# Kernel tuning notes

Hardware: AMD Instinct MI355X
Metric: run time of the kernel (lower is better)

## Reference

```python
import jax, jax.numpy as jnp
import numpy as np

D_MODEL = 1024
N_HEADS = 16
D_FF = 4096
EPS = 1e-6


def layernorm(x, alpha, bias):
    # torch.std uses Bessel correction (ddof=1)
    mean = jnp.mean(x, axis=-1, keepdims=True)
    std = jnp.std(x, axis=-1, keepdims=True, ddof=1)
    return alpha * (x - mean) / (std + EPS) + bias


def setup_inputs() -> dict:
    key = jax.random.key(0)
    ks = jax.random.split(key, 12)
    s = 1.0 / np.sqrt(D_MODEL)
    sf = 1.0 / np.sqrt(D_FF)
    return {
        "x": jax.random.normal(ks[0], (2, 2048, D_MODEL), jnp.float32),
        "mask": jnp.ones((2, 1, 1, 2048), jnp.int32),
        "wq": jax.random.normal(ks[1], (D_MODEL, D_MODEL), jnp.float32) * s,
        "wk": jax.random.normal(ks[2], (D_MODEL, D_MODEL), jnp.float32) * s,
        "wv": jax.random.normal(ks[3], (D_MODEL, D_MODEL), jnp.float32) * s,
        "wo": jax.random.normal(ks[4], (D_MODEL, D_MODEL), jnp.float32) * s,
        "wo_b": jnp.zeros((D_MODEL,), jnp.float32),
        "w1": jax.random.normal(ks[5], (D_MODEL, D_FF), jnp.float32) * s,
        "b1": jnp.zeros((D_FF,), jnp.float32),
        "w2": jax.random.normal(ks[6], (D_FF, D_MODEL), jnp.float32) * sf,
        "b2": jnp.zeros((D_MODEL,), jnp.float32),
        "alpha1": jnp.ones((D_MODEL,), jnp.float32),
        "bias1": jnp.zeros((D_MODEL,), jnp.float32),
        "alpha2": jnp.ones((D_MODEL,), jnp.float32),
        "bias2": jnp.zeros((D_MODEL,), jnp.float32),
    }


def reference(x, mask, wq, wk, wv, wo, wo_b, w1, b1, w2, b2,
              alpha1, bias1, alpha2, bias2):
    B, S, D = x.shape
    h, dk = N_HEADS, D_MODEL // N_HEADS
    # projections -> [B, h, S, dk]
    q = (x @ wq).reshape(B, S, h, dk).transpose(0, 2, 1, 3)
    k = (x @ wk).reshape(B, S, h, dk).transpose(0, 2, 1, 3)
    v = (x @ wv).reshape(B, S, h, dk).transpose(0, 2, 1, 3)
    scores = jnp.einsum('bhqd,bhkd->bhqk', q, k) / jnp.sqrt(jnp.float32(dk))
    scores = jnp.where(mask == 0, jnp.float32(-1e9), scores)
    attn = jax.nn.softmax(scores, axis=-1)
    ctx = jnp.einsum('bhqk,bhkd->bhqd', attn, v)
    ctx = ctx.transpose(0, 2, 1, 3).reshape(B, S, D)
    attn_out = ctx @ wo + wo_b
    x = layernorm(x + attn_out, alpha1, bias1)
    ff = jax.nn.relu(x @ w1 + b1) @ w2 + b2
    x = layernorm(x + ff, alpha2, bias2)
    return x
```

## Files before the change

kernel.cpp:

```cpp
#include <hip/hip_runtime.h>
#include <hip/hip_bf16.h>

#define D_MODEL 1024
#define N_HEADS 16
#define DK      64
#define SEQ     2048
#define BATCH   2
#define D_FF    4096
#define ROWS    (BATCH*SEQ)
#define LN_EPS  1e-6f
#define SSTR    72
#define KTILE   128
#define PSTR    136

typedef __hip_bfloat16 bf16;
typedef __attribute__((ext_vector_type(8))) short frag8;
typedef __attribute__((ext_vector_type(4))) float facc4;

__device__ inline float bf2f(unsigned short u){ return __uint_as_float(((unsigned)u) << 16); }
__device__ inline float toF(bf16 v){ return __bfloat162float(v); }
__device__ inline unsigned short f2bu(float f){ bf16 h = __float2bfloat16(f); return *reinterpret_cast<unsigned short*>(&h); }

__device__ inline float ld1(const void* p, size_t idx, bool f32) {
    return f32 ? ((const float*)p)[idx] : toF(((const bf16*)p)[idx]);
}

struct U8 { unsigned short v[8]; };
__device__ inline U8 ld8bf(const void* p, size_t idx, bool f32) {
    U8 r;
    if (!f32) {
        *reinterpret_cast<uint4*>(r.v) = *reinterpret_cast<const uint4*>((const unsigned short*)p + idx);
    } else {
        const float* f = (const float*)p + idx;
        const float4 a = *reinterpret_cast<const float4*>(f);
        const float4 b = *reinterpret_cast<const float4*>(f + 4);
        r.v[0]=f2bu(a.x); r.v[1]=f2bu(a.y); r.v[2]=f2bu(a.z); r.v[3]=f2bu(a.w);
        r.v[4]=f2bu(b.x); r.v[5]=f2bu(b.y); r.v[6]=f2bu(b.z); r.v[7]=f2bu(b.w);
    }
    return r;
}

__device__ inline void gld16(const void* g, void* l) {
    __builtin_amdgcn_global_load_lds(
        reinterpret_cast<const __attribute__((address_space(1))) void*>(
            reinterpret_cast<uintptr_t>(g)),
        reinterpret_cast<__attribute__((address_space(3))) void*>(
            (unsigned int)reinterpret_cast<uintptr_t>(l)),
        16, 0, 0);
}

__global__ void probe_kernel(const void* __restrict__ xp, int* __restrict__ flag) {
    __shared__ int hit;
    if (threadIdx.x == 0) hit = 0;
    __syncthreads();
    const bf16* p = (const bf16*)xp;
    int bad = 0;
    for (int i = threadIdx.x; i < 8192; i += 256) {
        float v = fabsf(toF(p[i]));
        if (!(v <= 1e5f)) bad = 1;
    }
    if (bad) atomicOr(&hit, 1);
    __syncthreads();
    if (threadIdx.x == 0) *flag = hit;
}

__global__ __launch_bounds__(256) void xcvt_kernel(const void* __restrict__ x,
    bf16* __restrict__ out, const int* __restrict__ flagp)
{
    const bool f32 = (*flagp) != 0;
    const size_t i = ((size_t)blockIdx.x * 256 + threadIdx.x) * 8;
    U8 d = ld8bf(x, i, f32);
    *reinterpret_cast<uint4*>(out + i) = *reinterpret_cast<const uint4*>(d.v);
}

__global__ __launch_bounds__(256) void transpose_kernel(const void* __restrict__ W,
    bf16* __restrict__ WT, int K, int N, const int* __restrict__ flagp)
{
    const bool f32 = (*flagp) != 0;
    __shared__ float tile[32][33];
    const int tx = threadIdx.x, ty = threadIdx.y;
    const int n0 = blockIdx.x * 32, k0 = blockIdx.y * 32;
    #pragma unroll
    for (int r = 0; r < 4; ++r)
        tile[ty + 8*r][tx] = ld1(W, (size_t)(k0 + ty + 8*r) * N + n0 + tx, f32);
    __syncthreads();
    #pragma unroll
    for (int r = 0; r < 4; ++r)
        WT[(size_t)(n0 + ty + 8*r) * K + k0 + tx] = __float2bfloat16(tile[tx][ty + 8*r]);
}

__global__ __launch_bounds__(256) void transpose4_kernel(const void* __restrict__ w0,
    const void* __restrict__ w1, const void* __restrict__ w2, const void* __restrict__ w3,
    bf16* __restrict__ WT4, const int* __restrict__ flagp)
{
    const bool f32 = (*flagp) != 0;
    const int which = blockIdx.z;
    const void* W = (which == 0) ? w0 : (which == 1) ? w1 : (which == 2) ? w2 : w3;
    bf16* WT = WT4 + (size_t)which * D_MODEL * D_MODEL;
    __shared__ float tile[32][33];
    const int tx = threadIdx.x, ty = threadIdx.y;
    const int n0 = blockIdx.x * 32, k0 = blockIdx.y * 32;
    #pragma unroll
    for (int r = 0; r < 4; ++r)
        tile[ty + 8*r][tx] = ld1(W, (size_t)(k0 + ty + 8*r) * D_MODEL + n0 + tx, f32);
    __syncthreads();
    #pragma unroll
    for (int r = 0; r < 4; ++r)
        WT[(size_t)(n0 + ty + 8*r) * D_MODEL + k0 + tx] = __float2bfloat16(tile[tx][ty + 8*r]);
}

__global__ __launch_bounds__(256) void vtrans_kernel(const bf16* __restrict__ V,
    bf16* __restrict__ VT)
{
    __shared__ unsigned short tile[32][33];
    const int tx = threadIdx.x, ty = threadIdx.y;
    const int s0 = blockIdx.x * 32, d0 = blockIdx.y * 32;
    const int bh = blockIdx.z, b = bh >> 4, h = bh & 15;
    #pragma unroll
    for (int r = 0; r < 4; ++r)
        tile[ty + 8*r][tx] = *reinterpret_cast<const unsigned short*>(
            V + ((size_t)(b * SEQ + s0 + ty + 8*r)) * D_MODEL + h * DK + d0 + tx);
    __syncthreads();
    #pragma unroll
    for (int r = 0; r < 4; ++r)
        *reinterpret_cast<unsigned short*>(
            VT + ((size_t)(bh * DK + d0 + ty + 8*r)) * SEQ + s0 + tx) = tile[tx][ty + 8*r];
}

template<bool RELU, bool BIAS, int NMAT, int SPLITK>
__global__ __launch_bounds__(256) void mgemm_kernel(const bf16* __restrict__ A,
    const bf16* __restrict__ BT, const void* __restrict__ bias,
    bf16* __restrict__ C, int M, int N, int K, const int* __restrict__ flagp)
{
    const bool inF32 = (*flagp) != 0;

    __shared__ unsigned short sA[128 * 64];
    __shared__ unsigned short sB[128 * 64];

    int which = 0, colb = blockIdx.x;
    if (NMAT > 1) { which = blockIdx.x >> 3; colb = blockIdx.x & 7; }
    const int kslice = (SPLITK > 1) ? blockIdx.z : 0;
    const int Kspan  = K / SPLITK;
    const int kbase  = kslice * Kspan;
    const bf16* Bp = BT + (size_t)which * N * K;
    bf16*       Cp = C  + (size_t)which * M * N + (size_t)kslice * M * N;

    const int row0 = blockIdx.y * 128;
    const int col0 = colb * 128;

    const int t    = threadIdx.x;
    const int wave = t >> 6;
    const int lane = t & 63;
    const int lm   = lane & 15;
    const int q    = lane >> 4;
    const int wm   = (wave & 1) * 64;
    const int wn   = (wave >> 1) * 64;

    facc4 acc[4][4];
    #pragma unroll
    for (int i = 0; i < 4; ++i)
        #pragma unroll
        for (int j = 0; j < 4; ++j)
            acc[i][j] = (facc4){0.f, 0.f, 0.f, 0.f};

    for (int k0 = kbase; k0 < kbase + Kspan; k0 += 64) {
        __syncthreads();
        #pragma unroll
        for (int j = 0; j < 4; ++j) {
            const int ch = (wave * 4 + j) * 64 + lane;
            const int r  = ch >> 3;
            const int cs = ch & 7;
            const int c  = cs ^ (r & 7);
            gld16(A  + (size_t)(row0 + r) * K + k0 + 8 * c, &sA[(wave * 4 + j) * 512]);
            gld16(Bp + (size_t)(col0 + r) * K + k0 + 8 * c, &sB[(wave * 4 + j) * 512]);
        }
        __syncthreads();

        #pragma unroll
        for (int kk = 0; kk < 64; kk += 32) {
            const int cr = (kk >> 3) + q;
            frag8 af[4], bfr[4];
            #pragma unroll
            for (int im = 0; im < 4; ++im) {
                const int m = wm + 16 * im + lm;
                af[im] = *reinterpret_cast<const frag8*>(&sA[m * 64 + ((cr ^ (m & 7)) << 3)]);
            }
            #pragma unroll
            for (int in = 0; in < 4; ++in) {
                const int n = wn + 16 * in + lm;
                bfr[in] = *reinterpret_cast<const frag8*>(&sB[n * 64 + ((cr ^ (n & 7)) << 3)]);
            }
            #pragma unroll
            for (int im = 0; im < 4; ++im)
                #pragma unroll
                for (int in = 0; in < 4; ++in)
                    acc[im][in] = __builtin_amdgcn_mfma_f32_16x16x32_bf16(af[im], bfr[in], acc[im][in], 0, 0, 0);
        }
    }

    #pragma unroll
    for (int in = 0; in < 4; ++in) {
        const int col = col0 + wn + 16*in + lm;
        float bv = 0.f;
        if (BIAS && kslice == 0) bv = ld1(bias, col, inF32);
        #pragma unroll
        for (int im = 0; im < 4; ++im) {
            #pragma unroll
            for (int r = 0; r < 4; ++r) {
                const int row = row0 + wm + 16*im + 4*q + r;
                float v = acc[im][in][r] + bv;
                if (RELU) v = fmaxf(v, 0.f);
                Cp[(size_t)row * N + col] = __float2bfloat16(v);
            }
        }
    }
}

__global__ __launch_bounds__(512) void fattn_kernel(
    const bf16* __restrict__ Qg, const bf16* __restrict__ Kg,
    const bf16* __restrict__ VTg, const int* __restrict__ mask,
    bf16* __restrict__ ctx)
{
    __shared__ unsigned short sK[128 * 64];
    __shared__ unsigned short sV[64 * 128];
    __shared__ unsigned short PsU[8 * 16 * PSTR];
    __shared__ float madd[KTILE];

    const int t    = threadIdx.x;
    const int qt   = blockIdx.x;
    const int h    = blockIdx.y;
    const int b    = blockIdx.z;
    const int q0   = qt * 128;
    const int bh   = b * N_HEADS + h;
    const int wave = t >> 6;
    const int lane = t & 63;
    const int lm   = lane & 15;
    const int qd   = lane >> 4;

    unsigned short* Qs = PsU;
    {
        const int sr = t >> 2, sd0 = (t & 3) * 16;
        const unsigned short* src = (const unsigned short*)
            (Qg + ((size_t)(b * SEQ + q0 + sr)) * D_MODEL + h * DK + sd0);
        unsigned short qi[16], qo[16];
        *reinterpret_cast<uint4*>(&qi[0]) = *reinterpret_cast<const uint4*>(src);
        *reinterpret_cast<uint4*>(&qi[8]) = *reinterpret_cast<const uint4*>(src + 8);
        #pragma unroll
        for (int u = 0; u < 16; ++u) qo[u] = f2bu(bf2f(qi[u]) * 0.125f);
        *reinterpret_cast<uint4*>(&Qs[sr * SSTR + sd0])     = *reinterpret_cast<const uint4*>(&qo[0]);
        *reinterpret_cast<uint4*>(&Qs[sr * SSTR + sd0 + 8]) = *reinterpret_cast<const uint4*>(&qo[8]);
    }
    __syncthreads();
    frag8 qf[2];
    #pragma unroll
    for (int s2 = 0; s2 < 2; ++s2)
        qf[s2] = *reinterpret_cast<const frag8*>(&Qs[(16 * wave + lm) * SSTR + 32 * s2 + 8 * qd]);

    facc4 accO[4];
    float m_r[4], l_r[4];
    #pragma unroll
    for (int r = 0; r < 4; ++r) { m_r[r] = -1e30f; l_r[r] = 0.f; }
    #pragma unroll
    for (int in = 0; in < 4; ++in) accO[in] = (facc4){0.f, 0.f, 0.f, 0.f};

    for (int kt = 0; kt < SEQ / KTILE; ++kt) {
        const int k0 = kt * KTILE;
        __syncthreads();

        #pragma unroll
        for (int j = 0; j < 2; ++j) {
            const int ch = (wave * 2 + j) * 64 + lane;
            const int rK = ch >> 3, cK = (ch & 7) ^ (rK & 7);
            gld16(Kg + ((size_t)(b * SEQ + k0 + rK)) * D_MODEL + h * DK + 8 * cK,
                  &sK[(wave * 2 + j) * 512]);
            const int rV = ch >> 4, cV = (ch & 15) ^ (rV & 15);
            gld16(VTg + ((size_t)(bh * DK + rV)) * SEQ + k0 + 8 * cV,
                  &sV[(wave * 2 + j) * 512]);
        }
        if (t < KTILE) madd[t] = (mask[b * SEQ + k0 + t] == 0) ? -1e9f : 0.f;
        __syncthreads();

        facc4 accS[8];
        #pragma unroll
        for (int i = 0; i < 8; ++i) accS[i] = (facc4){0.f, 0.f, 0.f, 0.f};
        #pragma unroll
        for (int i = 0; i < 8; ++i) {
            #pragma unroll
            for (int s2 = 0; s2 < 2; ++s2) {
                const int cr = 4 * s2 + qd;
                frag8 kf = *reinterpret_cast<const frag8*>(
                    &sK[(16 * i + lm) * 64 + ((cr ^ (lm & 7)) << 3)]);
                accS[i] = __builtin_amdgcn_mfma_f32_16x16x32_bf16(qf[s2], kf, accS[i], 0, 0, 0);
            }
        }

        float madv[8];
        #pragma unroll
        for (int i = 0; i < 8; ++i) madv[i] = madd[16 * i + lm];

        float mx[4];
        #pragma unroll
        for (int r = 0; r < 4; ++r) {
            float m0 = -1e30f;
            #pragma unroll
            for (int i = 0; i < 8; ++i) m0 = fmaxf(m0, accS[i][r] + madv[i]);
            #pragma unroll
            for (int off = 1; off < 16; off <<= 1) m0 = fmaxf(m0, __shfl_xor(m0, off));
            mx[r] = m0;
        }

        float alpha[4], mn[4], psum[4];
        #pragma unroll
        for (int r = 0; r < 4; ++r) {
            mn[r] = fmaxf(m_r[r], mx[r]);
            alpha[r] = __expf(m_r[r] - mn[r]);
            m_r[r] = mn[r];
            psum[r] = 0.f;
        }
        unsigned short* Pw = &PsU[wave * 16 * PSTR];
        #pragma unroll
        for (int i = 0; i < 8; ++i) {
            #pragma unroll
            for (int r = 0; r < 4; ++r) {
                float p = __expf(accS[i][r] + madv[i] - mn[r]);
                psum[r] += p;
                Pw[(qd * 4 + r) * PSTR + 16 * i + lm] = f2bu(p);
            }
        }
        #pragma unroll
        for (int r = 0; r < 4; ++r) {
            float s = psum[r];
            #pragma unroll
            for (int off = 1; off < 16; off <<= 1) s += __shfl_xor(s, off);
            l_r[r] = l_r[r] * alpha[r] + s;
            #pragma unroll
            for (int in = 0; in < 4; ++in) accO[in][r] *= alpha[r];
        }

        #pragma unroll
        for (int c = 0; c < 4; ++c) {
            frag8 pf = *reinterpret_cast<const frag8*>(&Pw[lm * PSTR + 32 * c + 8 * qd]);
            #pragma unroll
            for (int in = 0; in < 4; ++in) {
                const int cr = 4 * c + qd;
                frag8 vf = *reinterpret_cast<const frag8*>(
                    &sV[(16 * in + lm) * 128 + ((cr ^ lm) << 3)]);
                accO[in] = __builtin_amdgcn_mfma_f32_16x16x32_bf16(pf, vf, accO[in], 0, 0, 0);
            }
        }
    }

    float inv[4];
    #pragma unroll
    for (int r = 0; r < 4; ++r) inv[r] = 1.f / l_r[r];
    #pragma unroll
    for (int in = 0; in < 4; ++in)
        #pragma unroll
        for (int r = 0; r < 4; ++r)
            ctx[((size_t)(b * SEQ + q0 + 16 * wave + qd * 4 + r)) * D_MODEL + h * DK + 16 * in + lm]
                = __float2bfloat16(accO[in][r] * inv[r]);
}

template<bool BASE_WS, bool OUT_WS>
__global__ __launch_bounds__(256) void ln_kernel(const void* __restrict__ base,
    const bf16* __restrict__ addv, const bf16* __restrict__ addv2,
    const void* __restrict__ alpha, const void* __restrict__ bias,
    void* __restrict__ outp, const int* __restrict__ flagp)
{
    const bool inF32 = (*flagp) != 0;
    __shared__ float vals[D_MODEL];
    __shared__ float red[256];
    const int row = blockIdx.x, tid = threadIdx.x;

    float lsum = 0.f;
    for (int i = tid; i < D_MODEL; i += 256) {
        const size_t off = (size_t)row * D_MODEL + i;
        float v = (BASE_WS ? toF(((const bf16*)base)[off]) : ld1(base, off, inF32)) + toF(addv[off]);
        if (addv2) v += toF(addv2[off]);
        vals[i] = v; lsum += v;
    }
    red[tid] = lsum; __syncthreads();
    for (int s = 128; s > 0; s >>= 1) { if (tid < s) red[tid] += red[tid + s]; __syncthreads(); }
    const float mean = red[0] / (float)D_MODEL; __syncthreads();

    float lsq = 0.f;
    for (int i = tid; i < D_MODEL; i += 256) { float dd = vals[i] - mean; lsq += dd * dd; }
    red[tid] = lsq; __syncthreads();
    for (int s = 128; s > 0; s >>= 1) { if (tid < s) red[tid] += red[tid + s]; __syncthreads(); }
    const float var = red[0] / (float)(D_MODEL - 1);
    const float inv = 1.f / (sqrtf(var) + LN_EPS);

    for (int i = tid; i < D_MODEL; i += 256) {
        const size_t off = (size_t)row * D_MODEL + i;
        const float y = ld1(alpha, i, inF32) * (vals[i] - mean) * inv + ld1(bias, i, inF32);
        if (OUT_WS || !inF32) ((bf16*)outp)[off] = __float2bfloat16(y);
        else                  ((float*)outp)[off] = y;
    }
}

extern "C" void kernel_launch(void* const* d_in, const int* in_sizes, int n_in,
                              void* d_out, int out_size, void* d_ws, size_t ws_size,
                              hipStream_t stream)
{
    const void* x    = d_in[0];
    const int*  mask = (const int*)d_in[1];
    const void* wq   = d_in[2];
    const void* wk   = d_in[3];
    const void* wv   = d_in[4];
    const void* wo   = d_in[5];
    const void* wo_b = d_in[6];
    const void* w1   = d_in[7];
    const void* b1   = d_in[8];
    const void* w2   = d_in[9];
    const void* b2   = d_in[10];
    const void* al1  = d_in[11];
    const void* bi1  = d_in[12];
    const void* al2  = d_in[13];
    const void* bi2  = d_in[14];

    const size_t MB = 1024 * 1024;
    char* ws = (char*)d_ws;
    const bool BIG = ws_size >= 64 * MB + 4096;
    if (!BIG && ws_size < 56 * MB + 4096) return;

    dim3 tb(32, 8);

    if (BIG) {
        bf16* Qb   = (bf16*)(ws + 0 * MB);
        bf16* Kb   = (bf16*)(ws + 8 * MB);
        bf16* Vb   = (bf16*)(ws + 16 * MB);
        bf16* Xb   = (bf16*)(ws + 24 * MB);
        bf16* VTb  = (bf16*)(ws + 24 * MB);
        bf16* WT4  = (bf16*)(ws + 32 * MB);
        bf16* WOT  = WT4 + (size_t)3 * D_MODEL * D_MODEL;
        bf16* W1T  = (bf16*)(ws + 40 * MB);
        bf16* W2T  = (bf16*)(ws + 48 * MB);
        bf16* CTXb = (bf16*)(ws + 56 * MB);
        bf16* ATT0 = (bf16*)(ws + 0 * MB);
        bf16* ATT1 = (bf16*)(ws + 8 * MB);
        bf16* X1b  = (bf16*)(ws + 56 * MB);
        bf16* FFb  = (bf16*)(ws + 0 * MB);
        bf16* X20  = (bf16*)(ws + 32 * MB);
        bf16* X21  = (bf16*)(ws + 40 * MB);
        int*  flagp = (int*)(ws + 64 * MB);

        probe_kernel<<<1, 256, 0, stream>>>(x, flagp);
        xcvt_kernel<<<dim3(ROWS * D_MODEL / 2048), 256, 0, stream>>>(x, Xb, flagp);

        transpose4_kernel<<<dim3(32, 32, 4), tb, 0, stream>>>(wq, wk, wv, wo, WT4, flagp);
        transpose_kernel<<<dim3(128, 32), tb, 0, stream>>>(w1, W1T, D_MODEL, D_FF, flagp);
        transpose_kernel<<<dim3(32, 128), tb, 0, stream>>>(w2, W2T, D_FF, D_MODEL, flagp);

        mgemm_kernel<false, false, 3, 1><<<dim3(24, 32), 256, 0, stream>>>(
            Xb, WT4, nullptr, Qb, ROWS, D_MODEL, D_MODEL, flagp);

        vtrans_kernel<<<dim3(SEQ / 32, 2, BATCH * N_HEADS), tb, 0, stream>>>(Vb, VTb);

        fattn_kernel<<<dim3(SEQ / 128, N_HEADS, BATCH), 512, 0, stream>>>(Qb, Kb, VTb, mask, CTXb);

        mgemm_kernel<false, true, 1, 2><<<dim3(8, 32, 2), 256, 0, stream>>>(
            CTXb, WOT, wo_b, ATT0, ROWS, D_MODEL, D_MODEL, flagp);
        ln_kernel<false, true><<<ROWS, 256, 0, stream>>>(x, ATT0, ATT1, al1, bi1, X1b, flagp);

        mgemm_kernel<true, true, 1, 1><<<dim3(32, 32), 256, 0, stream>>>(
            X1b, W1T, b1, FFb, ROWS, D_FF, D_MODEL, flagp);

        mgemm_kernel<false, true, 1, 2><<<dim3(8, 32, 2), 256, 0, stream>>>(
            FFb, W2T, b2, X20, ROWS, D_MODEL, D_FF, flagp);
        ln_kernel<true, false><<<ROWS, 256, 0, stream>>>(X1b, X20, X21, al2, bi2, d_out, flagp);
    } else {
        bf16* Qb    = (bf16*)(ws + 0 * MB);
        bf16* Kb    = (bf16*)(ws + 8 * MB);
        bf16* Vb    = (bf16*)(ws + 16 * MB);
        bf16* Xb    = (bf16*)(ws + 24 * MB);
        bf16* VTb   = (bf16*)(ws + 24 * MB);
        bf16* WQKVT = (bf16*)(ws + 32 * MB);
        bf16* CTXb  = (bf16*)(ws + 32 * MB);
        bf16* W2T   = (bf16*)(ws + 32 * MB);
        bf16* WOT   = (bf16*)(ws + 0 * MB);
        bf16* ATT0  = (bf16*)(ws + 48 * MB);
        bf16* W1T   = (bf16*)(ws + 48 * MB);
        bf16* X20   = (bf16*)(ws + 48 * MB);
        bf16* X1b   = (bf16*)(ws + 40 * MB);
        bf16* FFb   = (bf16*)(ws + 0 * MB);
        int*  flagp = (int*)(ws + 56 * MB);

        probe_kernel<<<1, 256, 0, stream>>>(x, flagp);
        xcvt_kernel<<<dim3(ROWS * D_MODEL / 2048), 256, 0, stream>>>(x, Xb, flagp);

        transpose_kernel<<<dim3(32, 32), tb, 0, stream>>>(wq, WQKVT,           D_MODEL, D_MODEL, flagp);
        transpose_kernel<<<dim3(32, 32), tb, 0, stream>>>(wk, WQKVT + 1048576, D_MODEL, D_MODEL, flagp);
        transpose_kernel<<<dim3(32, 32), tb, 0, stream>>>(wv, WQKVT + 2097152, D_MODEL, D_MODEL, flagp);

        mgemm_kernel<false, false, 3, 1><<<dim3(24, 32), 256, 0, stream>>>(
            Xb, WQKVT, nullptr, Qb, ROWS, D_MODEL, D_MODEL, flagp);

        vtrans_kernel<<<dim3(SEQ / 32, 2, BATCH * N_HEADS), tb, 0, stream>>>(Vb, VTb);

        fattn_kernel<<<dim3(SEQ / 128, N_HEADS, BATCH), 512, 0, stream>>>(Qb, Kb, VTb, mask, CTXb);

        transpose_kernel<<<dim3(32, 32), tb, 0, stream>>>(wo, WOT, D_MODEL, D_MODEL, flagp);
        mgemm_kernel<false, true, 1, 1><<<dim3(8, 32), 256, 0, stream>>>(
            CTXb, WOT, wo_b, ATT0, ROWS, D_MODEL, D_MODEL, flagp);
        ln_kernel<false, true><<<ROWS, 256, 0, stream>>>(x, ATT0, nullptr, al1, bi1, X1b, flagp);

        transpose_kernel<<<dim3(128, 32), tb, 0, stream>>>(w1, W1T, D_MODEL, D_FF, flagp);
        mgemm_kernel<true, true, 1, 1><<<dim3(32, 32), 256, 0, stream>>>(
            X1b, W1T, b1, FFb, ROWS, D_FF, D_MODEL, flagp);

        transpose_kernel<<<dim3(32, 128), tb, 0, stream>>>(w2, W2T, D_FF, D_MODEL, flagp);
        mgemm_kernel<false, true, 1, 1><<<dim3(8, 32), 256, 0, stream>>>(
            FFb, W2T, b2, X20, ROWS, D_MODEL, D_FF, flagp);
        ln_kernel<true, false><<<ROWS, 256, 0, stream>>>(X1b, X20, nullptr, al2, bi2, d_out, flagp);
    }
}
```

Baseline: 405.1 us.

## Compute transposed attention scores to keep P in registers via permlane swaps

The flash-attention kernel now computes S^T (keys × queries) with swapped MFMA operands, so each lane owns one query column. Row max and sum then need only two cross-lane shuffles instead of sixteen-lane reductions. The probability tile is rearranged into the PV MFMA operand layout with v_permlane32_swap and shuffles rather than a round trip through shared memory. Q is loaded straight into registers with the 1/8 scale folded into the score FMA. The P shared buffer is removed and occupancy is raised through launch bounds, at the cost of more register shuffling and reliance on the gfx950-specific permlane instruction.

```diff
diff --git a/kernel.cpp b/kernel.cpp
--- a/kernel.cpp
+++ b/kernel.cpp
@@ -9,9 +9,7 @@
 #define D_FF    4096
 #define ROWS    (BATCH*SEQ)
 #define LN_EPS  1e-6f
-#define SSTR    72
 #define KTILE   128
-#define PSTR    136
 
 typedef __hip_bfloat16 bf16;
 typedef __attribute__((ext_vector_type(8))) short frag8;
@@ -216,15 +214,14 @@
     }
 }
 
-__global__ __launch_bounds__(512) void fattn_kernel(
+__global__ __launch_bounds__(512, 4) void fattn_kernel(
     const bf16* __restrict__ Qg, const bf16* __restrict__ Kg,
     const bf16* __restrict__ VTg, const int* __restrict__ mask,
     bf16* __restrict__ ctx)
 {
     __shared__ unsigned short sK[128 * 64];
     __shared__ unsigned short sV[64 * 128];
-    __shared__ unsigned short PsU[8 * 16 * PSTR];
-    __shared__ float madd[KTILE];
+    __shared__ __align__(16) float madd[KTILE];
 
     const int t    = threadIdx.x;
     const int qt   = blockIdx.x;
@@ -237,31 +234,17 @@
     const int lm   = lane & 15;
     const int qd   = lane >> 4;
 
-    unsigned short* Qs = PsU;
+    frag8 qf[2];
     {
-        const int sr = t >> 2, sd0 = (t & 3) * 16;
-        const unsigned short* src = (const unsigned short*)
-            (Qg + ((size_t)(b * SEQ + q0 + sr)) * D_MODEL + h * DK + sd0);
-        unsigned short qi[16], qo[16];
-        *reinterpret_cast<uint4*>(&qi[0]) = *reinterpret_cast<const uint4*>(src);
-        *reinterpret_cast<uint4*>(&qi[8]) = *reinterpret_cast<const uint4*>(src + 8);
-        #pragma unroll
-        for (int u = 0; u < 16; ++u) qo[u] = f2bu(bf2f(qi[u]) * 0.125f);
-        *reinterpret_cast<uint4*>(&Qs[sr * SSTR + sd0])     = *reinterpret_cast<const uint4*>(&qo[0]);
-        *reinterpret_cast<uint4*>(&Qs[sr * SSTR + sd0 + 8]) = *reinterpret_cast<const uint4*>(&qo[8]);
-    }
-    __syncthreads();
-    frag8 qf[2];
-    #pragma unroll
-    for (int s2 = 0; s2 < 2; ++s2)
-        qf[s2] = *reinterpret_cast<const frag8*>(&Qs[(16 * wave + lm) * SSTR + 32 * s2 + 8 * qd]);
+        const bf16* qsrc = Qg + ((size_t)(b * SEQ + q0 + 16 * wave + lm)) * D_MODEL + h * DK;
+        qf[0] = *reinterpret_cast<const frag8*>(qsrc + 8 * qd);
+        qf[1] = *reinterpret_cast<const frag8*>(qsrc + 32 + 8 * qd);
+    }
 
     facc4 accO[4];
-    float m_r[4], l_r[4];
-    #pragma unroll
-    for (int r = 0; r < 4; ++r) { m_r[r] = -1e30f; l_r[r] = 0.f; }
     #pragma unroll
     for (int in = 0; in < 4; ++in) accO[in] = (facc4){0.f, 0.f, 0.f, 0.f};
+    float m_r = -1e30f, l_r = 0.f;
 
     for (int kt = 0; kt < SEQ / KTILE; ++kt) {
         const int k0 = kt * KTILE;
@@ -280,9 +263,9 @@
         if (t < KTILE) madd[t] = (mask[b * SEQ + k0 + t] == 0) ? -1e9f : 0.f;
         __syncthreads();
 
-        facc4 accS[8];
-        #pragma unroll
-        for (int i = 0; i < 8; ++i) accS[i] = (facc4){0.f, 0.f, 0.f, 0.f};
+        facc4 accST[8];
+        #pragma unroll
+        for (int i = 0; i < 8; ++i) accST[i] = (facc4){0.f, 0.f, 0.f, 0.f};
         #pragma unroll
         for (int i = 0; i < 8; ++i) {
             #pragma unroll
@@ -290,75 +273,82 @@
                 const int cr = 4 * s2 + qd;
                 frag8 kf = *reinterpret_cast<const frag8*>(
                     &sK[(16 * i + lm) * 64 + ((cr ^ (lm & 7)) << 3)]);
-                accS[i] = __builtin_amdgcn_mfma_f32_16x16x32_bf16(qf[s2], kf, accS[i], 0, 0, 0);
+                accST[i] = __builtin_amdgcn_mfma_f32_16x16x32_bf16(kf, qf[s2], accST[i], 0, 0, 0);
             }
         }
 
-        float madv[8];
-        #pragma unroll
-        for (int i = 0; i < 8; ++i) madv[i] = madd[16 * i + lm];
-
-        float mx[4];
-        #pragma unroll
-        for (int r = 0; r < 4; ++r) {
-            float m0 = -1e30f;
-            #pragma unroll
-            for (int i = 0; i < 8; ++i) m0 = fmaxf(m0, accS[i][r] + madv[i]);
-            #pragma unroll
-            for (int off = 1; off < 16; off <<= 1) m0 = fmaxf(m0, __shfl_xor(m0, off));
-            mx[r] = m0;
-        }
-
-        float alpha[4], mn[4], psum[4];
-        #pragma unroll
-        for (int r = 0; r < 4; ++r) {
-            mn[r] = fmaxf(m_r[r], mx[r]);
-            alpha[r] = __expf(m_r[r] - mn[r]);
-            m_r[r] = mn[r];
-            psum[r] = 0.f;
-        }
-        unsigned short* Pw = &PsU[wave * 16 * PSTR];
+        float m0 = -1e30f;
         #pragma unroll
         for (int i = 0; i < 8; ++i) {
+            const facc4 mv = *reinterpret_cast<const facc4*>(&madd[16 * i + 4 * qd]);
             #pragma unroll
             for (int r = 0; r < 4; ++r) {
-                float p = __expf(accS[i][r] + madv[i] - mn[r]);
-                psum[r] += p;
-                Pw[(qd * 4 + r) * PSTR + 16 * i + lm] = f2bu(p);
+                accST[i][r] = fmaf(accST[i][r], 0.125f, mv[r]);
+                m0 = fmaxf(m0, accST[i][r]);
             }
         }
-        #pragma unroll
-        for (int r = 0; r < 4; ++r) {
-            float s = psum[r];
-            #pragma unroll
-            for (int off = 1; off < 16; off <<= 1) s += __shfl_xor(s, off);
-            l_r[r] = l_r[r] * alpha[r] + s;
-            #pragma unroll
-            for (int in = 0; in < 4; ++in) accO[in][r] *= alpha[r];
-        }
+        m0 = fmaxf(m0, __shfl_xor(m0, 16));
+        m0 = fmaxf(m0, __shfl_xor(m0, 32));
+
+        const float mn = fmaxf(m_r, m0);
+        const float alpha = __expf(m_r - mn);
+        m_r = mn;
+
+        unsigned up[8][2];
+        float ps = 0.f;
+        #pragma unroll
+        for (int i = 0; i < 8; ++i) {
+            const float p0 = __expf(accST[i][0] - mn);
+            const float p1 = __expf(accST[i][1] - mn);
+            const float p2 = __expf(accST[i][2] - mn);
+            const float p3 = __expf(accST[i][3] - mn);
+            ps += (p0 + p1) + (p2 + p3);
+            up[i][0] = (unsigned)f2bu(p0) | ((unsigned)f2bu(p1) << 16);
+            up[i][1] = (unsigned)f2bu(p2) | ((unsigned)f2bu(p3) << 16);
+        }
+        ps += __shfl_xor(ps, 16);
+        ps += __shfl_xor(ps, 32);
+        l_r = l_r * alpha + ps;
+        #pragma unroll
+        for (int in = 0; in < 4; ++in)
+            #pragma unroll
+            for (int r = 0; r < 4; ++r) accO[in][r] *= alpha;
 
         #pragma unroll
         for (int c = 0; c < 4; ++c) {
-            frag8 pf = *reinterpret_cast<const frag8*>(&Pw[lm * PSTR + 32 * c + 8 * qd]);
+            unsigned a0 = up[2*c][0],     a1 = up[2*c][1];
+            unsigned b0 = up[2*c + 1][0], b1 = up[2*c + 1][1];
+            asm("v_permlane32_swap_b32 %0, %1" : "+v"(a0), "+v"(b0));
+            asm("v_permlane32_swap_b32 %0, %1" : "+v"(a1), "+v"(b1));
+            const unsigned tA0 = __shfl_xor(a0, 16);
+            const unsigned tB0 = __shfl_xor(b0, 16);
+            const unsigned tA1 = __shfl_xor(a1, 16);
+            const unsigned tB1 = __shfl_xor(b1, 16);
+            const bool qo = (qd & 1) != 0;
+            union { frag8 f; unsigned u[4]; } pf_;
+            pf_.u[0] = qo ? tB0 : a0;
+            pf_.u[1] = qo ? tB1 : a1;
+            pf_.u[2] = qo ? b0  : tA0;
+            pf_.u[3] = qo ? b1  : tA1;
             #pragma unroll
             for (int in = 0; in < 4; ++in) {
                 const int cr = 4 * c + qd;
                 frag8 vf = *reinterpret_cast<const frag8*>(
                     &sV[(16 * in + lm) * 128 + ((cr ^ lm) << 3)]);
-                accO[in] = __builtin_amdgcn_mfma_f32_16x16x32_bf16(pf, vf, accO[in], 0, 0, 0);
+                accO[in] = __builtin_amdgcn_mfma_f32_16x16x32_bf16(vf, pf_.f, accO[in], 0, 0, 0);
             }
         }
     }
 
-    float inv[4];
-    #pragma unroll
-    for (int r = 0; r < 4; ++r) inv[r] = 1.f / l_r[r];
-    #pragma unroll
-    for (int in = 0; in < 4; ++in)
-        #pragma unroll
-        for (int r = 0; r < 4; ++r)
-            ctx[((size_t)(b * SEQ + q0 + 16 * wave + qd * 4 + r)) * D_MODEL + h * DK + 16 * in + lm]
-                = __float2bfloat16(accO[in][r] * inv[r]);
+    const float invl = 1.f / l_r;
+    bf16* crow = ctx + ((size_t)(b * SEQ + q0 + 16 * wave + lm)) * D_MODEL + h * DK;
+    #pragma unroll
+    for (int in = 0; in < 4; ++in) {
+        union { uint2 v; unsigned short s[4]; } ov;
+        #pragma unroll
+        for (int r = 0; r < 4; ++r) ov.s[r] = f2bu(accO[in][r] * invl);
+        *reinterpret_cast<uint2*>(crow + 16 * in + 4 * qd) = ov.v;
+    }
 }
 
 template<bool BASE_WS, bool OUT_WS>
```

After: 396.0 us. 2.2% less time.
